# Optimization experiments

Measured on AMD Instinct MI355X. Metric: run time of the kernel, lower is better.

Reference implementation:

```python
import jax, jax.numpy as jnp
import numpy as np

DIM = 256
MIN_HZ = 0.5
MAX_HZ = 4.0
SEQ_LEN = 65536


def setup_inputs() -> dict:
    key = jax.random.key(0)
    k1, k2 = jax.random.split(key)
    # raw per-step observation probabilities (positive; renormalized inside the layer)
    probs = jax.random.uniform(k1, (SEQ_LEN, DIM), dtype=jnp.float32)
    # transition prior (positive weights; per-step normalization makes scale irrelevant)
    transition_prior = jax.random.uniform(k2, (DIM, DIM), dtype=jnp.float32)
    return {"probs": probs, "transition_prior": transition_prior}


def _bins(dim):
    # _bin_hr_bpm(i) = min_hz*60 + (max_hz-min_hz)*60*i/dim
    i = jnp.arange(dim, dtype=jnp.float32)
    return MIN_HZ * 60.0 + (MAX_HZ - MIN_HZ) * 60.0 * i / dim


def reference(probs, transition_prior):
    """Online sum-product belief propagation (PriorLayer, online=True, return_probs=True,
    uncert='entropy'). probs: (S, dim). Returns (prior_probs (S, dim), uncertainty (S,))."""
    dim = probs.shape[1]
    bins = _bins(dim)

    def step(state, p_t):
        p_prior = transition_prior @ state          # (dim,) matvec
        p_new = p_prior * p_t                       # elementwise with observation
        state = p_new / jnp.sum(p_new)              # renormalize belief
        return state, state

    init_state = jnp.ones((dim,), dtype=probs.dtype) / dim
    _, prior_probs = jax.lax.scan(step, init_state, probs)   # (S, dim)

    uncertainty = -jnp.sum(prior_probs * jnp.log(prior_probs + 1e-10), axis=1)  # entropy (S,)
    return prior_probs, uncertainty
```

## Files before the change

### kernel.cpp

```cpp
#include <hip/hip_runtime.h>
#include <hip/hip_bf16.h>
#include <stdint.h>


#define DIM   256
#define SEQ   65536
#define G     16
#define CLEN  16
#define NBLK  (SEQ / (G * CLEN))
#define BURN  6
#define STEPS (BURN + CLEN)
#define NW    4
#define TPB   (NW * 64)
#define PGP   17

typedef short bf16x8 __attribute__((ext_vector_type(8)));
typedef float f32x4  __attribute__((ext_vector_type(4)));
typedef float f32x2  __attribute__((ext_vector_type(2)));

static __device__ __forceinline__ unsigned short f2bf(float x) {
  __hip_bfloat16 h = __float2bfloat16(x);
  return *reinterpret_cast<unsigned short*>(&h);
}

static __device__ __forceinline__ void lds_barrier() {
  asm volatile("s_waitcnt lgkmcnt(0)" ::: "memory");
  __builtin_amdgcn_s_barrier();
}

__global__ __launch_bounds__(TPB, 1)
void prior_scan_kernel(const float* __restrict__ probs,
                       const float* __restrict__ tp,
                       float* __restrict__ out) {
  __shared__ __attribute__((aligned(16))) short SB[2][8][64][8];
  __shared__ __attribute__((aligned(16))) f32x2 pZL[2][G][PGP];

  const int tid  = threadIdx.x;
  const int w    = tid >> 6;
  const int lane = tid & 63;
  const int n    = lane & 15;
  const int quad = lane >> 4;
  const int g    = blockIdx.x * G + n;

  bf16x8 A[4][8];
#pragma unroll
  for (int rt = 0; rt < 4; rt++) {
    const int row = w * 64 + rt * 16 + n;
#pragma unroll
    for (int kb = 0; kb < 8; kb++) {
      const float* p = tp + row * DIM + kb * 32 + quad * 8;
      f32x4 f0 = *reinterpret_cast<const f32x4*>(p);
      f32x4 f1 = *reinterpret_cast<const f32x4*>(p + 4);
      bf16x8 a;
#pragma unroll
      for (int j = 0; j < 4; j++) {
        a[j]     = (short)f2bf(f0[j]);
        a[4 + j] = (short)f2bf(f1[j]);
      }
      A[rt][kb] = a;
    }
  }

  {
    ushort4 u; u.x = u.y = u.z = u.w = (unsigned short)0x3B80;
    ushort4* dst = reinterpret_cast<ushort4*>(&SB[0][0][0][0]) + tid * 4;
    dst[0] = u; dst[1] = u; dst[2] = u; dst[3] = u;
  }

  auto loadp = [&](int s, int rt, bool clamp) -> f32x4 {
    int t = g * CLEN - BURN + s;
    if (clamp && t < 0) t = 0;
    return *reinterpret_cast<const f32x4*>(
        probs + (size_t)t * DIM + w * 64 + rt * 16 + quad * 4);
  };

  f32x4 pf[2][4];
#pragma unroll
  for (int rt = 0; rt < 4; rt++) {
    pf[0][rt] = loadp(0, rt, true);
    pf[1][rt] = loadp(1, rt, true);
  }

  __syncthreads();

  float qp[4][4];

  auto matvec = [&](int cur, float (&q)[4][4]) {
    bf16x8 B[8];
#pragma unroll
    for (int kb = 0; kb < 8; kb++)
      B[kb] = *reinterpret_cast<const bf16x8*>(&SB[cur][kb][lane][0]);
    f32x4 aE[4], aO[4];
#pragma unroll
    for (int rt = 0; rt < 4; rt++) {
      aE[rt] = f32x4{0.f, 0.f, 0.f, 0.f};
      aO[rt] = f32x4{0.f, 0.f, 0.f, 0.f};
    }
#pragma unroll
    for (int kb = 0; kb < 8; kb += 2) {
#pragma unroll
      for (int rt = 0; rt < 4; rt++) {
        aE[rt] = __builtin_amdgcn_mfma_f32_16x16x32_bf16(A[rt][kb],     B[kb],     aE[rt], 0, 0, 0);
        aO[rt] = __builtin_amdgcn_mfma_f32_16x16x32_bf16(A[rt][kb + 1], B[kb + 1], aO[rt], 0, 0, 0);
      }
    }
#pragma unroll
    for (int rt = 0; rt < 4; rt++)
#pragma unroll
      for (int v = 0; v < 4; v++)
        q[rt][v] = (aE[rt][v] + aO[rt][v]) * pf[cur][rt][v];
  };

  auto write_state = [&](int nxt, const float (&q)[4][4]) {
#pragma unroll
    for (int rt = 0; rt < 4; rt++) {
      ushort4 sp;
      sp.x = f2bf(q[rt][0] * 0.015625f);
      sp.y = f2bf(q[rt][1] * 0.015625f);
      sp.z = f2bf(q[rt][2] * 0.015625f);
      sp.w = f2bf(q[rt][3] * 0.015625f);
      *reinterpret_cast<ushort4*>(
          &SB[nxt][w * 2 + (rt >> 1)][((rt & 1) * 2 + (quad >> 1)) * 16 + n]
             [(quad & 1) * 4]) = sp;
    }
  };

  auto finalize = [&](int pbuf, int e1) {
    float Z = 0.f, L = 0.f;
#pragma unroll
    for (int j = 0; j < 8; j++) {
      f32x4 r = *reinterpret_cast<const f32x4*>(&pZL[pbuf][n][j * 2]);
      Z += r[0] + r[2];
      L += r[1] + r[3];
    }
    const float zi = __builtin_amdgcn_rcpf(Z);
    const int t1 = g * CLEN + (e1 - BURN);
#pragma unroll
    for (int rt = 0; rt < 4; rt++) {
      f32x4 o;
#pragma unroll
      for (int v = 0; v < 4; v++) o[v] = qp[rt][v] * zi;
      *reinterpret_cast<f32x4*>(
          out + (size_t)t1 * DIM + w * 64 + rt * 16 + quad * 4) = o;
    }
    if (tid < 16)
      out[(size_t)SEQ * DIM + t1] = __logf(Z) - L * zi;
  };

  auto burn_body = [&](int e, int cur, int nxt) {
    float q[4][4];
    matvec(cur, q);
#pragma unroll
    for (int rt = 0; rt < 4; rt++)
      pf[cur][rt] = loadp(e + 2, rt, true);
    const int t = g * CLEN - BURN + e;
    if (t < 0) {
      ushort4 sp;
      sp.x = sp.y = sp.z = sp.w = (unsigned short)0x3B80;
#pragma unroll
      for (int rt = 0; rt < 4; rt++)
        *reinterpret_cast<ushort4*>(
            &SB[nxt][w * 2 + (rt >> 1)][((rt & 1) * 2 + (quad >> 1)) * 16 + n]
               [(quad & 1) * 4]) = sp;
    } else {
      write_state(nxt, q);
    }
    lds_barrier();
  };

  auto main_body = [&](int e, int cur, int nxt) {
    float q[4][4];
    matvec(cur, q);
    int ps = e + 2; if (ps > STEPS - 1) ps = STEPS - 1;
#pragma unroll
    for (int rt = 0; rt < 4; rt++)
      pf[cur][rt] = loadp(ps, rt, false);
    write_state(nxt, q);

    float sz = 0.f, sl = 0.f;
#pragma unroll
    for (int rt = 0; rt < 4; rt++)
#pragma unroll
      for (int v = 0; v < 4; v++) {
        float qq = q[rt][v];
        sz += qq;
        sl += qq * __logf(qq + 1e-30f);
      }
    pZL[cur][n][w * 4 + quad] = f32x2{sz, sl};

    if (e > BURN) finalize(nxt, e - 1);

#pragma unroll
    for (int rt = 0; rt < 4; rt++)
#pragma unroll
      for (int v = 0; v < 4; v++) qp[rt][v] = q[rt][v];
    lds_barrier();
  };

#pragma clang loop unroll(disable)
  for (int e = 0; e < BURN; e += 2) {
    burn_body(e, 0, 1);
    burn_body(e + 1, 1, 0);
  }
#pragma clang loop unroll(disable)
  for (int e = BURN; e < STEPS; e += 2) {
    main_body(e, 0, 1);
    main_body(e + 1, 1, 0);
  }

  finalize((STEPS - 1) & 1, STEPS - 1);
}

extern "C" void kernel_launch(void* const* d_in, const int* in_sizes, int n_in,
                              void* d_out, int out_size, void* d_ws, size_t ws_size,
                              hipStream_t stream) {
  const float* probs = (const float*)d_in[0];
  const float* tp    = (const float*)d_in[1];
  float* out         = (float*)d_out;

  hipLaunchKernelGGL(prior_scan_kernel, dim3(NBLK), dim3(TPB), 0, stream,
                     probs, tp, out);
}
```

Before: 136.0 us.

## Stage probs loads and output stores through LDS for coalesced row access

Observation rows are now loaded by each wavefront as full contiguous 1 KB rows and transposed through an LDS buffer, instead of each lane gathering scattered 16-byte pieces from 16 different chains. Outputs are likewise written to an LDS tile and streamed back as whole contiguous rows one step later. The goal is better coalescing of global memory traffic. In exchange it adds LDS traffic, needs about 88 KB of dynamic shared memory, and adds an extra barrier at the end.

```diff
diff --git a/kernel.cpp b/kernel.cpp
--- a/kernel.cpp
+++ b/kernel.cpp
@@ -13,6 +13,13 @@
 #define NW    4
 #define TPB   (NW * 64)
 #define PGP   17
+#define PROW  264
+
+#define SB_OFF  0
+#define PT_OFF  16384
+#define OT_OFF  50176
+#define ZL_OFF  83968
+#define LDS_BYTES 88320
 
 typedef short bf16x8 __attribute__((ext_vector_type(8)));
 typedef float f32x4  __attribute__((ext_vector_type(4)));
@@ -32,15 +39,29 @@
 void prior_scan_kernel(const float* __restrict__ probs,
                        const float* __restrict__ tp,
                        float* __restrict__ out) {
-  __shared__ __attribute__((aligned(16))) short SB[2][8][64][8];
-  __shared__ __attribute__((aligned(16))) f32x2 pZL[2][G][PGP];
+  extern __shared__ __align__(16) char lds_raw[];
+  short* SBb = reinterpret_cast<short*>(lds_raw + SB_OFF);
+  float* PTb = reinterpret_cast<float*>(lds_raw + PT_OFF);
+  float* OTb = reinterpret_cast<float*>(lds_raw + OT_OFF);
+  f32x2* ZLb = reinterpret_cast<f32x2*>(lds_raw + ZL_OFF);
 
   const int tid  = threadIdx.x;
   const int w    = tid >> 6;
   const int lane = tid & 63;
   const int n    = lane & 15;
   const int quad = lane >> 4;
-  const int g    = blockIdx.x * G + n;
+  const int cbase = blockIdx.x * G;
+  const int g    = cbase + n;
+
+  auto SB = [&](int buf, int kb, int l, int j) -> short* {
+    return SBb + (((buf * 8 + kb) * 64 + l) * 8 + j);
+  };
+  auto PT = [&](int buf, int nn, int i) -> float* {
+    return PTb + ((buf * 16 + nn) * PROW + i);
+  };
+  auto OT = [&](int buf, int nn, int i) -> float* {
+    return OTb + ((buf * 16 + nn) * PROW + i);
+  };
 
   bf16x8 A[4][8];
 #pragma unroll
@@ -63,24 +84,35 @@
 
   {
     ushort4 u; u.x = u.y = u.z = u.w = (unsigned short)0x3B80;
-    ushort4* dst = reinterpret_cast<ushort4*>(&SB[0][0][0][0]) + tid * 4;
+    ushort4* dst = reinterpret_cast<ushort4*>(SBb) + tid * 4;
     dst[0] = u; dst[1] = u; dst[2] = u; dst[3] = u;
   }
 
-  auto loadp = [&](int s, int rt, bool clamp) -> f32x4 {
-    int t = g * CLEN - BURN + s;
-    if (clamp && t < 0) t = 0;
-    return *reinterpret_cast<const f32x4*>(
-        probs + (size_t)t * DIM + w * 64 + rt * 16 + quad * 4);
-  };
-
-  f32x4 pf[2][4];
-#pragma unroll
-  for (int rt = 0; rt < 4; rt++) {
-    pf[0][rt] = loadp(0, rt, true);
-    pf[1][rt] = loadp(1, rt, true);
-  }
-
+  f32x4 P4[4];
+  auto load_rows = [&](int s) {
+#pragma unroll
+    for (int j = 0; j < 4; j++) {
+      int t = (cbase + 4 * w + j) * CLEN - BURN + s;
+      if (t < 0) t = 0;
+      P4[j] = *reinterpret_cast<const f32x4*>(
+          probs + (size_t)t * DIM + lane * 4);
+    }
+  };
+
+  {
+    f32x4 tmp[4];
+#pragma unroll
+    for (int j = 0; j < 4; j++) {
+      int t = (cbase + 4 * w + j) * CLEN - BURN;
+      if (t < 0) t = 0;
+      tmp[j] = *reinterpret_cast<const f32x4*>(
+          probs + (size_t)t * DIM + lane * 4);
+    }
+#pragma unroll
+    for (int j = 0; j < 4; j++)
+      *reinterpret_cast<f32x4*>(PT(0, 4 * w + j, lane * 4)) = tmp[j];
+    load_rows(1);
+  }
   __syncthreads();
 
   float qp[4][4];
@@ -89,7 +121,12 @@
     bf16x8 B[8];
 #pragma unroll
     for (int kb = 0; kb < 8; kb++)
-      B[kb] = *reinterpret_cast<const bf16x8*>(&SB[cur][kb][lane][0]);
+      B[kb] = *reinterpret_cast<const bf16x8*>(SB(cur, kb, lane, 0));
+    f32x4 P[4];
+#pragma unroll
+    for (int rt = 0; rt < 4; rt++)
+      P[rt] = *reinterpret_cast<const f32x4*>(
+          PT(cur, n, w * 64 + rt * 16 + quad * 4));
     f32x4 aE[4], aO[4];
 #pragma unroll
     for (int rt = 0; rt < 4; rt++) {
@@ -108,7 +145,15 @@
     for (int rt = 0; rt < 4; rt++)
 #pragma unroll
       for (int v = 0; v < 4; v++)
-        q[rt][v] = (aE[rt][v] + aO[rt][v]) * pf[cur][rt][v];
+        q[rt][v] = (aE[rt][v] + aO[rt][v]) * P[rt][v];
+  };
+
+  auto stagePT = [&](int e, int nxt) {
+#pragma unroll
+    for (int j = 0; j < 4; j++)
+      *reinterpret_cast<f32x4*>(PT(nxt, 4 * w + j, lane * 4)) = P4[j];
+    int s2 = e + 2; if (s2 > STEPS - 1) s2 = STEPS - 1;
+    load_rows(s2);
   };
 
   auto write_state = [&](int nxt, const float (&q)[4][4]) {
@@ -120,39 +165,49 @@
       sp.z = f2bf(q[rt][2] * 0.015625f);
       sp.w = f2bf(q[rt][3] * 0.015625f);
       *reinterpret_cast<ushort4*>(
-          &SB[nxt][w * 2 + (rt >> 1)][((rt & 1) * 2 + (quad >> 1)) * 16 + n]
-             [(quad & 1) * 4]) = sp;
+          SB(nxt, w * 2 + (rt >> 1),
+             ((rt & 1) * 2 + (quad >> 1)) * 16 + n, (quad & 1) * 4)) = sp;
     }
   };
 
   auto finalize = [&](int pbuf, int e1) {
     float Z = 0.f, L = 0.f;
+    const f32x2* zl = ZLb + (pbuf * 16 + n) * PGP;
 #pragma unroll
     for (int j = 0; j < 8; j++) {
-      f32x4 r = *reinterpret_cast<const f32x4*>(&pZL[pbuf][n][j * 2]);
+      f32x4 r = *reinterpret_cast<const f32x4*>(zl + j * 2);
       Z += r[0] + r[2];
       L += r[1] + r[3];
     }
     const float zi = __builtin_amdgcn_rcpf(Z);
-    const int t1 = g * CLEN + (e1 - BURN);
 #pragma unroll
     for (int rt = 0; rt < 4; rt++) {
       f32x4 o;
 #pragma unroll
       for (int v = 0; v < 4; v++) o[v] = qp[rt][v] * zi;
       *reinterpret_cast<f32x4*>(
-          out + (size_t)t1 * DIM + w * 64 + rt * 16 + quad * 4) = o;
-    }
-    if (tid < 16)
+          OT(pbuf, n, w * 64 + rt * 16 + quad * 4)) = o;
+    }
+    if (tid < 16) {
+      const int t1 = g * CLEN + (e1 - BURN);
       out[(size_t)SEQ * DIM + t1] = __logf(Z) - L * zi;
+    }
+  };
+
+  auto stream_out = [&](int pbuf, int e1) {
+#pragma unroll
+    for (int j = 0; j < 4; j++) {
+      const int nn = 4 * w + j;
+      f32x4 v = *reinterpret_cast<const f32x4*>(OT(pbuf, nn, lane * 4));
+      const int t1 = (cbase + nn) * CLEN + (e1 - BURN);
+      *reinterpret_cast<f32x4*>(out + (size_t)t1 * DIM + lane * 4) = v;
+    }
   };
 
   auto burn_body = [&](int e, int cur, int nxt) {
     float q[4][4];
     matvec(cur, q);
-#pragma unroll
-    for (int rt = 0; rt < 4; rt++)
-      pf[cur][rt] = loadp(e + 2, rt, true);
+    stagePT(e, nxt);
     const int t = g * CLEN - BURN + e;
     if (t < 0) {
       ushort4 sp;
@@ -160,8 +215,8 @@
 #pragma unroll
       for (int rt = 0; rt < 4; rt++)
         *reinterpret_cast<ushort4*>(
-            &SB[nxt][w * 2 + (rt >> 1)][((rt & 1) * 2 + (quad >> 1)) * 16 + n]
-               [(quad & 1) * 4]) = sp;
+            SB(nxt, w * 2 + (rt >> 1),
+               ((rt & 1) * 2 + (quad >> 1)) * 16 + n, (quad & 1) * 4)) = sp;
     } else {
       write_state(nxt, q);
     }
@@ -171,10 +226,7 @@
   auto main_body = [&](int e, int cur, int nxt) {
     float q[4][4];
     matvec(cur, q);
-    int ps = e + 2; if (ps > STEPS - 1) ps = STEPS - 1;
-#pragma unroll
-    for (int rt = 0; rt < 4; rt++)
-      pf[cur][rt] = loadp(ps, rt, false);
+    stagePT(e, nxt);
     write_state(nxt, q);
 
     float sz = 0.f, sl = 0.f;
@@ -186,8 +238,9 @@
         sz += qq;
         sl += qq * __logf(qq + 1e-30f);
       }
-    pZL[cur][n][w * 4 + quad] = f32x2{sz, sl};
-
+    *(ZLb + (cur * 16 + n) * PGP + (w * 4 + quad)) = f32x2{sz, sl};
+
+    if (e >= BURN + 2) stream_out(cur, e - 2);
     if (e > BURN) finalize(nxt, e - 1);
 
 #pragma unroll
@@ -208,7 +261,10 @@
     main_body(e + 1, 1, 0);
   }
 
+  stream_out((STEPS - 2) & 1, STEPS - 2);
   finalize((STEPS - 1) & 1, STEPS - 1);
+  lds_barrier();
+  stream_out((STEPS - 1) & 1, STEPS - 1);
 }
 
 extern "C" void kernel_launch(void* const* d_in, const int* in_sizes, int n_in,
@@ -218,6 +274,13 @@
   const float* tp    = (const float*)d_in[1];
   float* out         = (float*)d_out;
 
-  hipLaunchKernelGGL(prior_scan_kernel, dim3(NBLK), dim3(TPB), 0, stream,
-                     probs, tp, out);
-}
+  static bool configured = false;
+  if (!configured) {
+    hipFuncSetAttribute(reinterpret_cast<const void*>(prior_scan_kernel),
+                        hipFuncAttributeMaxDynamicSharedMemorySize, LDS_BYTES);
+    configured = true;
+  }
+
+  hipLaunchKernelGGL(prior_scan_kernel, dim3(NBLK), dim3(TPB), LDS_BYTES,
+                     stream, probs, tp, out);
+}
```

New measurement: 142.0 us. 1.04x slower.
